# Optimization experiments

Measured on AMD Instinct MI355X. Metric: run time of the kernel, lower is better.

The kernel has to match this reference:

```python
import jax, jax.numpy as jnp
import numpy as np

N, D = 8192, 1024


def setup_inputs() -> dict:
    key = jax.random.key(0)
    k1, k2 = jax.random.split(key)
    x = jax.random.normal(k1, (N, D), dtype=jnp.float32)
    # scale weight like a trained linear layer (~1/sqrt(D)) so softmax isn't fully saturated
    W = jax.random.normal(k2, (D, D), dtype=jnp.float32) * (1.0 / np.sqrt(D))
    b = jnp.zeros((D,), dtype=jnp.float32)
    recency_weight = jnp.full((1,), -0.5, dtype=jnp.float32)  # nn.Parameter init in source
    return {"x": x, "W": W, "b": b, "recency_weight": recency_weight}


def reference(x, W, b, recency_weight):
    # linear + relu
    x_proj = jax.nn.relu(x @ W.T + b)          # [N, D]
    # tied self-matmul
    scores = x_proj @ x_proj.T                  # [N, N]
    n = x.shape[0]
    idx = jnp.arange(n)
    # causal mask: upper triangle strictly above diagonal (use_current_timestep=True)
    upper = idx[None, :] > idx[:, None]         # [N, N] bool
    scores = jnp.where(upper, -jnp.inf, scores)
    # recency bias: toeplitz |i - j|, zeroed on masked (upper) part, scaled by recency_weight
    dist = jnp.abs(idx[:, None] - idx[None, :]).astype(scores.dtype)
    recency = recency_weight[0] * jnp.where(upper, 0.0, dist)
    scores = scores + recency
    return jax.nn.softmax(scores, axis=1)       # [N, N] lower-triangular attention
```

## Files before the change

kernel.cpp:

```cpp
#include <hip/hip_runtime.h>
#include <hip/hip_fp8.h>
#include <math.h>

#define NR 8192
#define DIM 1024
#define BK 32

typedef __attribute__((ext_vector_type(4))) float f32x4;

static __device__ __forceinline__ unsigned short f2bf(float f) {
  unsigned int u = __float_as_uint(f);
  u += 0x7fffu + ((u >> 16) & 1u);
  return (unsigned short)(u >> 16);
}

static __device__ __forceinline__ float bf2f(unsigned short u) {
  return __uint_as_float(((unsigned int)u) << 16);
}

static __device__ __forceinline__ unsigned char f2fp8(float f) {
  __hip_fp8_e4m3 q(f);
  return *reinterpret_cast<const unsigned char*>(&q);
}

static __device__ __forceinline__ void gload_lds16(const void* g, void* lds) {
  __builtin_amdgcn_global_load_lds(
      (const __attribute__((address_space(1))) unsigned int*)g,
      (__attribute__((address_space(3))) unsigned int*)lds, 16, 0, 0);
}

__global__ __launch_bounds__(256) void zerok(float* __restrict__ p, int n) {
  int i = blockIdx.x * 256 + threadIdx.x;
  if (i < n) p[i] = 0.0f;
}

__global__ __launch_bounds__(256) void cvt_fp8(const float* __restrict__ in,
                                               unsigned char* __restrict__ outp,
                                               int n8) {
  int i = blockIdx.x * 256 + threadIdx.x;
  if (i < n8) {
    float4 a = ((const float4*)in)[2 * i];
    float4 b = ((const float4*)in)[2 * i + 1];
    union { unsigned char c[8]; uint2 u; } o;
    o.c[0] = f2fp8(a.x); o.c[1] = f2fp8(a.y); o.c[2] = f2fp8(a.z); o.c[3] = f2fp8(a.w);
    o.c[4] = f2fp8(b.x); o.c[5] = f2fp8(b.y); o.c[6] = f2fp8(b.z); o.c[7] = f2fp8(b.w);
    ((uint2*)outp)[i] = o.u;
  }
}

static __device__ __forceinline__ void gemm_core_fp8(const unsigned char* A,
                                                     const unsigned char* B,
                                                     int m0, int n0,
                                                     unsigned char* S,
                                                     f32x4 acc[4][4]) {
  const int tid  = threadIdx.x;
  const int lane = tid & 63;
  const int wave = tid >> 6;
  const int wr = wave >> 1, wc = wave & 1;
  const int li = lane & 15, g = lane >> 4;
  const int ar  = wave * 32 + (lane >> 1);
  const int acl = (lane & 1) ^ ((ar >> 2) & 1);
  const int pc = ((g >> 1) ^ ((li >> 2) & 1)) * 16 + (g & 1) * 8;

#define ISSUE_TILE8(t_)                                                             \
  do {                                                                              \
    const int kt_ = (t_) * BK;                                                      \
    unsigned char* buf_ = S + ((t_) & 3) * 8192;                                    \
    gload_lds16(A + (size_t)(m0 + ar) * DIM + kt_ + acl * 16,                       \
                buf_ + wave * 1024);                                                \
    gload_lds16(B + (size_t)(n0 + ar) * DIM + kt_ + acl * 16,                       \
                buf_ + 4096 + wave * 1024);                                         \
  } while (0)

  ISSUE_TILE8(0);
  ISSUE_TILE8(1);
  ISSUE_TILE8(2);

  for (int t = 0; t < DIM / BK; ++t) {
    if (t <= DIM / BK - 3)      asm volatile("s_waitcnt vmcnt(4)" ::: "memory");
    else if (t == DIM / BK - 2) asm volatile("s_waitcnt vmcnt(2)" ::: "memory");
    else                        asm volatile("s_waitcnt vmcnt(0)" ::: "memory");
    __builtin_amdgcn_s_barrier();

    const unsigned char* Ab = S + (t & 3) * 8192;
    const unsigned char* Bb = Ab + 4096;
    long av[4], bv[4];
#pragma unroll
    for (int m = 0; m < 4; ++m)
      av[m] = *(const long*)(Ab + (wr * 64 + m * 16 + li) * 32 + pc);
#pragma unroll
    for (int n = 0; n < 4; ++n)
      bv[n] = *(const long*)(Bb + (wc * 64 + n * 16 + li) * 32 + pc);
    asm volatile("s_waitcnt lgkmcnt(0)" ::: "memory");
    if (t + 3 < DIM / BK) ISSUE_TILE8(t + 3);
#pragma unroll
    for (int m = 0; m < 4; ++m)
#pragma unroll
      for (int n = 0; n < 4; ++n)
        acc[m][n] = __builtin_amdgcn_mfma_f32_16x16x32_fp8_fp8(av[m], bv[n], acc[m][n], 0, 0, 0);
  }
#undef ISSUE_TILE8
}

__global__ __launch_bounds__(256) void gemm1_relu(const unsigned char* __restrict__ Xq,
                                                  const unsigned char* __restrict__ Wq,
                                                  const float* __restrict__ bias,
                                                  unsigned char* __restrict__ XPq,
                                                  float* __restrict__ diag) {
  __shared__ unsigned char S[32768];
  const int m0 = blockIdx.y * 128, n0 = blockIdx.x * 128;
  f32x4 acc[4][4] = {};
  gemm_core_fp8(Xq, Wq, m0, n0, S, acc);

  const int lane = threadIdx.x & 63, wave = threadIdx.x >> 6;
  const int wr = wave >> 1, wc = wave & 1, g = lane >> 4, li = lane & 15;
  float bv[4];
#pragma unroll
  for (int n = 0; n < 4; ++n) bv[n] = bias[n0 + wc * 64 + n * 16 + li];
#pragma unroll
  for (int m = 0; m < 4; ++m) {
#pragma unroll
    for (int r = 0; r < 4; ++r) {
      int row = m0 + wr * 64 + m * 16 + g * 4 + r;
      float ds = 0.0f;
#pragma unroll
      for (int n = 0; n < 4; ++n) {
        int col = n0 + wc * 64 + n * 16 + li;
        float v = fmaxf(acc[m][n][r] + bv[n], 0.0f);
        XPq[(size_t)row * DIM + col] = f2fp8(v);
        ds += v * v;
      }
#pragma unroll
      for (int off = 1; off < 16; off <<= 1) ds += __shfl_xor(ds, off);
      if (li == 0) atomicAdd(&diag[row], ds);
    }
  }
}

__global__ __launch_bounds__(256) void gemm2_scores(const unsigned char* __restrict__ XPq,
                                                    const float* __restrict__ rwp,
                                                    unsigned short* __restrict__ Pb,
                                                    const float* __restrict__ diag,
                                                    float* __restrict__ Lrow) {
  int t = ((int)blockIdx.x & 7) * 260 + ((int)blockIdx.x >> 3);
  int by = (int)((sqrtf(8.0f * (float)t + 1.0f) - 1.0f) * 0.5f);
  while ((by + 1) * (by + 2) / 2 <= t) ++by;
  while (by * (by + 1) / 2 > t) --by;
  const int bx = t - by * (by + 1) / 2;

  __shared__ unsigned char S[32768];
  const int m0 = by * 128, n0 = bx * 128;
  f32x4 acc[4][4] = {};
  gemm_core_fp8(XPq, XPq, m0, n0, S, acc);

  const float rw = rwp[0];
  const int lane = threadIdx.x & 63, wave = threadIdx.x >> 6;
  const int wr = wave >> 1, wc = wave & 1, g = lane >> 4, li = lane & 15;

#pragma unroll
  for (int m = 0; m < 4; ++m) {
#pragma unroll
    for (int r = 0; r < 4; ++r) {
      const int row = m0 + wr * 64 + m * 16 + g * 4 + r;
      const float dg = diag[row];
      float se = 0.0f;
#pragma unroll
      for (int n = 0; n < 4; ++n) {
        int col = n0 + wc * 64 + n * 16 + li;
        float v = acc[m][n][r];
        v = (col <= row) ? v + rw * (float)(row - col) : -INFINITY;
        float e = __expf(v - dg);
        unsigned short eb = f2bf(e);
        se += bf2f(eb);
        if (col <= row) Pb[(size_t)row * NR + col] = eb;
      }
#pragma unroll
      for (int off = 1; off < 16; off <<= 1) se += __shfl_xor(se, off);
      if (li == 0) atomicAdd(&Lrow[row], se);
    }
  }
}

__global__ __launch_bounds__(256) void normk(const unsigned short* __restrict__ Pb,
                                             float* __restrict__ out,
                                             const float* __restrict__ Lrow) {
  const size_t idx = (size_t)blockIdx.x * 256 + threadIdx.x;
  const int row = (int)(idx >> 11);
  const int j0 = (int)(idx & 2047) * 4;
  float4* p = (float4*)out + idx;
  if (j0 > row) {
    float4 z; z.x = 0.f; z.y = 0.f; z.z = 0.f; z.w = 0.f;
    *p = z;
    return;
  }
  const float sc = __builtin_amdgcn_rcpf(Lrow[row]);
  ushort4 q = *(const ushort4*)(Pb + (size_t)row * NR + j0);
  float4 o;
  o.x = bf2f(q.x) * sc;
  o.y = bf2f(q.y) * sc;
  o.z = bf2f(q.z) * sc;
  o.w = bf2f(q.w) * sc;
  if (j0 + 3 > row) {
    if (j0 + 1 > row) o.y = 0.f;
    if (j0 + 2 > row) o.z = 0.f;
    o.w = 0.f;
  }
  *p = o;
}

extern "C" void kernel_launch(void* const* d_in, const int* in_sizes, int n_in,
                              void* d_out, int out_size, void* d_ws, size_t ws_size,
                              hipStream_t stream) {
  const float* x  = (const float*)d_in[0];
  const float* W  = (const float*)d_in[1];
  const float* b  = (const float*)d_in[2];
  const float* rw = (const float*)d_in[3];
  float* out = (float*)d_out;

  char* ws = (char*)d_ws;
  unsigned char* Xq  = (unsigned char*)(ws);
  unsigned char* Wq  = (unsigned char*)(ws + (size_t)(8 << 20));
  unsigned char* XPq = (unsigned char*)(ws + (size_t)(18 << 20));
  float* diag = (float*)(ws + (size_t)(34 << 20));
  float* Lrow = (float*)(ws + (size_t)(34 << 20) + 32768);
  unsigned short* Pb = (unsigned short*)(ws + (size_t)(64 << 20));

  zerok<<<(2 * NR + 255) / 256, 256, 0, stream>>>(diag, 2 * NR);
  cvt_fp8<<<NR * DIM / 8 / 256, 256, 0, stream>>>(x, Xq, NR * DIM / 8);
  cvt_fp8<<<DIM * DIM / 8 / 256, 256, 0, stream>>>(W, Wq, DIM * DIM / 8);
  gemm1_relu<<<dim3(DIM / 128, NR / 128), 256, 0, stream>>>(Xq, Wq, b, XPq, diag);
  gemm2_scores<<<2080, 256, 0, stream>>>(XPq, rw, Pb, diag, Lrow);
  normk<<<(NR / 4) * (NR / 256), 256, 0, stream>>>(Pb, out, Lrow);
}
```

Baseline: 430.5 us.

## Quantize projected activations to int8 and store softmax numerators as fp8

Gemm1 now writes ReLU outputs as fixed-point int8 (scale 32, clamped at 127). The diagonal norms are computed from the quantized values. Gemm2 uses a new int8 MFMA core (16x16x64) with a three-stage LDS pipeline, and the unnormalized exponentials are stored as fp8 instead of bf16, halving the intermediate matrix traffic. The risks are precision loss from the fixed-point clamp and fp8 probabilities, and higher LDS use in gemm2, which may reduce occupancy.

Result: faster. 406.6 us (-5.6%).

```diff
diff --git a/kernel.cpp b/kernel.cpp
--- a/kernel.cpp
+++ b/kernel.cpp
@@ -7,6 +7,7 @@
 #define BK 32
 
 typedef __attribute__((ext_vector_type(4))) float f32x4;
+typedef __attribute__((ext_vector_type(4))) int   i32x4;
 
 static __device__ __forceinline__ unsigned short f2bf(float f) {
   unsigned int u = __float_as_uint(f);
@@ -14,13 +15,15 @@
   return (unsigned short)(u >> 16);
 }
 
-static __device__ __forceinline__ float bf2f(unsigned short u) {
-  return __uint_as_float(((unsigned int)u) << 16);
-}
-
 static __device__ __forceinline__ unsigned char f2fp8(float f) {
   __hip_fp8_e4m3 q(f);
   return *reinterpret_cast<const unsigned char*>(&q);
+}
+
+static __device__ __forceinline__ float fp82f(unsigned char c) {
+  __hip_fp8_e4m3 h;
+  h.__x = (__hip_fp8_storage_t)c;
+  return (float)h;
 }
 
 static __device__ __forceinline__ void gload_lds16(const void* g, void* lds) {
@@ -102,10 +105,69 @@
 #undef ISSUE_TILE8
 }
 
+static __device__ __forceinline__ void gemm_core_i8(const signed char* A,
+                                                    const signed char* B,
+                                                    int m0, int n0,
+                                                    signed char* S,
+                                                    i32x4 acc[4][4]) {
+  const int tid  = threadIdx.x;
+  const int lane = tid & 63;
+  const int wave = tid >> 6;
+  const int wr = wave >> 1, wc = wave & 1;
+  const int li = lane & 15, g = lane >> 4;
+  const int tr = tid >> 2;
+  const int c  = (tid & 3) ^ ((tr >> 1) & 3);
+  const int pco = (g ^ ((li >> 1) & 3)) * 16;
+
+#define ISSUE_I8(t_)                                                                \
+  do {                                                                              \
+    const int kt_ = (t_) * 64;                                                      \
+    signed char* buf_ = S + ((t_) % 3) * 16384;                                     \
+    gload_lds16(A + (size_t)(m0 + tr)      * DIM + kt_ + c * 16,                    \
+                buf_ + wave * 1024);                                                \
+    gload_lds16(A + (size_t)(m0 + 64 + tr) * DIM + kt_ + c * 16,                    \
+                buf_ + 4096 + wave * 1024);                                         \
+    gload_lds16(B + (size_t)(n0 + tr)      * DIM + kt_ + c * 16,                    \
+                buf_ + 8192 + wave * 1024);                                         \
+    gload_lds16(B + (size_t)(n0 + 64 + tr) * DIM + kt_ + c * 16,                    \
+                buf_ + 12288 + wave * 1024);                                        \
+  } while (0)
+
+  ISSUE_I8(0);
+  ISSUE_I8(1);
+  ISSUE_I8(2);
+
+  const int NT = DIM / 64;
+  for (int t = 0; t < NT; ++t) {
+    if (t <= NT - 3)      asm volatile("s_waitcnt vmcnt(8)" ::: "memory");
+    else if (t == NT - 2) asm volatile("s_waitcnt vmcnt(4)" ::: "memory");
+    else                  asm volatile("s_waitcnt vmcnt(0)" ::: "memory");
+    __builtin_amdgcn_s_barrier();
+
+    const signed char* Ab = S + (t % 3) * 16384;
+    const signed char* Bb = Ab + 8192;
+    i32x4 av[4], bv[4];
+#pragma unroll
+    for (int m = 0; m < 4; ++m)
+      av[m] = *(const i32x4*)(Ab + (wr * 64 + m * 16 + li) * 64 + pco);
+#pragma unroll
+    for (int n = 0; n < 4; ++n)
+      bv[n] = *(const i32x4*)(Bb + (wc * 64 + n * 16 + li) * 64 + pco);
+    asm volatile("s_waitcnt lgkmcnt(0)" ::: "memory");
+    if (t + 3 < NT) ISSUE_I8(t + 3);
+#pragma unroll
+    for (int m = 0; m < 4; ++m)
+#pragma unroll
+      for (int n = 0; n < 4; ++n)
+        acc[m][n] = __builtin_amdgcn_mfma_i32_16x16x64_i8(av[m], bv[n], acc[m][n], 0, 0, 0);
+  }
+#undef ISSUE_I8
+}
+
 __global__ __launch_bounds__(256) void gemm1_relu(const unsigned char* __restrict__ Xq,
                                                   const unsigned char* __restrict__ Wq,
                                                   const float* __restrict__ bias,
-                                                  unsigned char* __restrict__ XPq,
+                                                  signed char* __restrict__ XPi,
                                                   float* __restrict__ diag) {
   __shared__ unsigned char S[32768];
   const int m0 = blockIdx.y * 128, n0 = blockIdx.x * 128;
@@ -127,8 +189,11 @@
       for (int n = 0; n < 4; ++n) {
         int col = n0 + wc * 64 + n * 16 + li;
         float v = fmaxf(acc[m][n][r] + bv[n], 0.0f);
-        XPq[(size_t)row * DIM + col] = f2fp8(v);
-        ds += v * v;
+        int qv = __float2int_rn(v * 32.0f);
+        qv = min(qv, 127);
+        XPi[(size_t)row * DIM + col] = (signed char)qv;
+        float vq = (float)qv * (1.0f / 32.0f);
+        ds += vq * vq;
       }
 #pragma unroll
       for (int off = 1; off < 16; off <<= 1) ds += __shfl_xor(ds, off);
@@ -137,9 +202,9 @@
   }
 }
 
-__global__ __launch_bounds__(256) void gemm2_scores(const unsigned char* __restrict__ XPq,
+__global__ __launch_bounds__(256) void gemm2_scores(const signed char* __restrict__ XPi,
                                                     const float* __restrict__ rwp,
-                                                    unsigned short* __restrict__ Pb,
+                                                    unsigned char* __restrict__ P8,
                                                     const float* __restrict__ diag,
                                                     float* __restrict__ Lrow) {
   int t = ((int)blockIdx.x & 7) * 260 + ((int)blockIdx.x >> 3);
@@ -148,12 +213,13 @@
   while (by * (by + 1) / 2 > t) --by;
   const int bx = t - by * (by + 1) / 2;
 
-  __shared__ unsigned char S[32768];
+  __shared__ signed char S[49152];
   const int m0 = by * 128, n0 = bx * 128;
-  f32x4 acc[4][4] = {};
-  gemm_core_fp8(XPq, XPq, m0, n0, S, acc);
+  i32x4 acc[4][4] = {};
+  gemm_core_i8(XPi, XPi, m0, n0, S, acc);
 
   const float rw = rwp[0];
+  const float qs = 1.0f / 1024.0f;
   const int lane = threadIdx.x & 63, wave = threadIdx.x >> 6;
   const int wr = wave >> 1, wc = wave & 1, g = lane >> 4, li = lane & 15;
 
@@ -167,12 +233,12 @@
 #pragma unroll
       for (int n = 0; n < 4; ++n) {
         int col = n0 + wc * 64 + n * 16 + li;
-        float v = acc[m][n][r];
+        float v = (float)acc[m][n][r] * qs;
         v = (col <= row) ? v + rw * (float)(row - col) : -INFINITY;
         float e = __expf(v - dg);
-        unsigned short eb = f2bf(e);
-        se += bf2f(eb);
-        if (col <= row) Pb[(size_t)row * NR + col] = eb;
+        unsigned char eb = f2fp8(e);
+        se += fp82f(eb);
+        if (col <= row) P8[(size_t)row * NR + col] = eb;
       }
 #pragma unroll
       for (int off = 1; off < 16; off <<= 1) se += __shfl_xor(se, off);
@@ -181,7 +247,7 @@
   }
 }
 
-__global__ __launch_bounds__(256) void normk(const unsigned short* __restrict__ Pb,
+__global__ __launch_bounds__(256) void normk(const unsigned char* __restrict__ P8,
                                              float* __restrict__ out,
                                              const float* __restrict__ Lrow) {
   const size_t idx = (size_t)blockIdx.x * 256 + threadIdx.x;
@@ -194,12 +260,13 @@
     return;
   }
   const float sc = __builtin_amdgcn_rcpf(Lrow[row]);
-  ushort4 q = *(const ushort4*)(Pb + (size_t)row * NR + j0);
+  const unsigned char* q = P8 + (size_t)row * NR + j0;
+  unsigned int qw = *(const unsigned int*)q;
   float4 o;
-  o.x = bf2f(q.x) * sc;
-  o.y = bf2f(q.y) * sc;
-  o.z = bf2f(q.z) * sc;
-  o.w = bf2f(q.w) * sc;
+  o.x = fp82f((unsigned char)(qw      )) * sc;
+  o.y = fp82f((unsigned char)(qw >>  8)) * sc;
+  o.z = fp82f((unsigned char)(qw >> 16)) * sc;
+  o.w = fp82f((unsigned char)(qw >> 24)) * sc;
   if (j0 + 3 > row) {
     if (j0 + 1 > row) o.y = 0.f;
     if (j0 + 2 > row) o.z = 0.f;
@@ -220,15 +287,15 @@
   char* ws = (char*)d_ws;
   unsigned char* Xq  = (unsigned char*)(ws);
   unsigned char* Wq  = (unsigned char*)(ws + (size_t)(8 << 20));
-  unsigned char* XPq = (unsigned char*)(ws + (size_t)(18 << 20));
+  signed char*   XPi = (signed char*)(ws + (size_t)(18 << 20));
   float* diag = (float*)(ws + (size_t)(34 << 20));
   float* Lrow = (float*)(ws + (size_t)(34 << 20) + 32768);
-  unsigned short* Pb = (unsigned short*)(ws + (size_t)(64 << 20));
+  unsigned char* P8 = (unsigned char*)(ws + (size_t)(64 << 20));
 
   zerok<<<(2 * NR + 255) / 256, 256, 0, stream>>>(diag, 2 * NR);
   cvt_fp8<<<NR * DIM / 8 / 256, 256, 0, stream>>>(x, Xq, NR * DIM / 8);
   cvt_fp8<<<DIM * DIM / 8 / 256, 256, 0, stream>>>(W, Wq, DIM * DIM / 8);
-  gemm1_relu<<<dim3(DIM / 128, NR / 128), 256, 0, stream>>>(Xq, Wq, b, XPq, diag);
-  gemm2_scores<<<2080, 256, 0, stream>>>(XPq, rw, Pb, diag, Lrow);
-  normk<<<(NR / 4) * (NR / 256), 256, 0, stream>>>(Pb, out, Lrow);
-}
+  gemm1_relu<<<dim3(DIM / 128, NR / 128), 256, 0, stream>>>(Xq, Wq, b, XPi, diag);
+  gemm2_scores<<<2080, 256, 0, stream>>>(XPi, rw, P8, diag, Lrow);
+  normk<<<(NR / 4) * (NR / 256), 256, 0, stream>>>(P8, out, Lrow);
+}
```
